# Optimization experiments

Measured on AMD Instinct MI355X. Metric: run time of the kernel, lower is better.

The kernel has to match this reference:

```python
import jax, jax.numpy as jnp
import numpy as np

B, T, D, H = 8, 2048, 256, 4
HD = D // H                      # head dim = 64
SCALE = float(np.sqrt(HD))       # math.sqrt(hd)
EPS = 1e-5                       # nn.LayerNorm default
NEG = -1e9                       # stand-in for -inf; sparsemax output identical (0)


def setup_inputs() -> dict:
    key = jax.random.key(0)
    ks = jax.random.split(key, 8)
    x = jax.random.normal(ks[0], (B, T, D), dtype=jnp.float32)
    key_padding_mask = jax.random.bernoulli(ks[1], 0.15, (B, T))
    w = lambda k: jax.random.normal(k, (D, D), dtype=jnp.float32) * 0.02
    return {
        "x": x,
        "key_padding_mask": key_padding_mask,
        "Wq": w(ks[2]), "Wk": w(ks[3]), "Wv": w(ks[4]), "Wo": w(ks[5]),
        "gamma": jnp.ones((D,), jnp.float32),
        "beta": jnp.zeros((D,), jnp.float32),
    }


def sparsemax(z):
    # exact sort-based sparsemax over last axis (Martins & Astudillo 2016)
    n = z.shape[-1]
    zs = -jnp.sort(-z, axis=-1)                      # descending
    k = jnp.arange(1, n + 1, dtype=z.dtype)
    cum = jnp.cumsum(zs, axis=-1)
    support = (1.0 + k * zs) > cum                   # k in support
    ksel = jnp.sum(support, axis=-1, keepdims=True)  # support size >= 1
    cum_k = jnp.take_along_axis(cum, ksel - 1, axis=-1)
    tau = (cum_k - 1.0) / ksel.astype(z.dtype)
    return jnp.maximum(z - tau, 0.0)


def _split(y):  # (B,T,D) -> (B,H,T,hd)
    return y.reshape(B, T, H, HD).transpose(0, 2, 1, 3)


def reference(x, key_padding_mask, Wq, Wk, Wv, Wo, gamma, beta):
    Q = _split(x @ Wq.T)
    K = _split(x @ Wk.T)
    V = _split(x @ Wv.T)
    scores = jnp.einsum('bhqd,bhkd->bhqk', Q, K) / SCALE     # (B,H,T,T)
    scores = jnp.where(key_padding_mask[:, None, None, :], NEG, scores)
    A = sparsemax(scores)
    out = jnp.einsum('bhqk,bhkd->bhqd', A, V)                # (B,H,T,hd)
    out = out.transpose(0, 2, 1, 3).reshape(B, T, D)
    y = out @ Wo.T + x                                       # out-proj + residual
    mu = jnp.mean(y, axis=-1, keepdims=True)
    var = jnp.mean(jnp.square(y - mu), axis=-1, keepdims=True)
    return (y - mu) / jnp.sqrt(var + EPS) * gamma + beta
```

## Files before the change

kernel.cpp:

```cpp
#include <hip/hip_runtime.h>

typedef unsigned short ushort_t;
typedef unsigned char uchar_t;

using bf16x8 = __attribute__((ext_vector_type(8))) short;
using f32x4  = __attribute__((ext_vector_type(4))) float;
using h2     = __attribute__((ext_vector_type(2))) _Float16;
using h8     = __attribute__((ext_vector_type(8))) _Float16;
using hc2    = __attribute__((ext_vector_type(2))) __fp16;
using hc8    = __attribute__((ext_vector_type(8))) __fp16;

#define B_  8
#define T_  2048
#define D_  256
#define H_  4
#define HD_ 64
#define BH_ (B_*H_)
#define M_  (B_*T_)

#define NX_   ((size_t)M_*D_)
#define NW_   ((size_t)D_*D_)
#define NCONV (NX_ + 4*NW_)

__device__ __forceinline__ float bf2f(ushort_t u) {
    union { unsigned int i; float f; } v; v.i = ((unsigned int)u) << 16; return v.f;
}
__device__ __forceinline__ ushort_t f2bf(float f) {
    union { float f; unsigned int i; } v; v.f = f;
    unsigned int u = v.i;
    u += 0x7FFFu + ((u >> 16) & 1u);
    return (ushort_t)(u >> 16);
}
__device__ __forceinline__ h2 pkh(float lo, float hi) {
    union { hc2 a; h2 b; } u;
    u.a = __builtin_amdgcn_cvt_pkrtz(lo, hi);
    return u.b;
}
__device__ __forceinline__ float dot2(h2 a, h2 b, float c) {
    union { h2 h; hc2 c2; } ua, ub; ua.h = a; ub.h = b;
    return __builtin_amdgcn_fdot2(ua.c2, ub.c2, c, false);
}
__device__ __forceinline__ f32x4 mfma_f16(h8 a, h8 b, f32x4 c) {
    union { h8 h; hc8 c8; } ua, ub; ua.h = a; ub.h = b;
    return __builtin_amdgcn_mfma_f32_16x16x32_f16(ua.c8, ub.c8, c, 0, 0, 0);
}
__device__ __forceinline__ f32x4 mfma_bf16(bf16x8 a, bf16x8 b, f32x4 c) {
    return __builtin_amdgcn_mfma_f32_16x16x32_bf16(a, b, c, 0, 0, 0);
}
__device__ __forceinline__ int is_bf16_inputs(const void* gamma) {
    return ((const unsigned int*)gamma)[0] == 0x3F803F80u;
}
union h2u { unsigned int u; int i; h2 h; };
union hu1 { _Float16 h; ushort_t u; };

__global__ __launch_bounds__(256) void conv_mask_kernel(
        const void* __restrict__ x,
        const void* __restrict__ Wq, const void* __restrict__ Wk,
        const void* __restrict__ Wv, const void* __restrict__ Wo,
        const void* __restrict__ gamma, ushort_t* __restrict__ dst,
        const uchar_t* __restrict__ mraw, ushort_t* __restrict__ mout) {
    int isbf = is_bf16_inputs(gamma);
    int tid = threadIdx.x;

    if (blockIdx.x < 16) {
        __shared__ int f_or1, f_ornz, f_max, cls;
        if (tid == 0) { f_or1 = 0; f_ornz = 0; f_max = 0; }
        __syncthreads();
        int lor1 = 0, lornz = 0, lmax = 0;
        for (int i = tid * 16; i < tid * 16 + 16; ++i) {
            int v = mraw[i];
            lmax = max(lmax, v);
            if ((i & 3) == 1) lor1 |= v;
            if ((i & 3) != 0) lornz |= v;
        }
        atomicOr(&f_or1, lor1); atomicOr(&f_ornz, lornz); atomicMax(&f_max, lmax);
        __syncthreads();
        if (tid == 0) {
            int c;
            if (f_max == 0)      c = 0;
            else if (f_max <= 1) c = f_ornz ? 0 : 1;
            else                 c = f_or1 ? 2 : 3;
            cls = c;
        }
        __syncthreads();
        int c = cls;
        int base = blockIdx.x * 1024;
        for (int e = base + tid; e < base + 1024; e += 256) {
            int m;
            if (c == 0)      m = mraw[e] != 0;
            else if (c == 1) m = ((const int*)mraw)[e] != 0;
            else if (c == 2) m = ((const ushort_t*)mraw)[e] != 0;
            else             m = ((const float*)mraw)[e] != 0.0f;
            hu1 cv; cv.h = m ? (_Float16)(-30000.0f) : (_Float16)0.0f;
            mout[e] = cv.u;
        }
    }

    size_t e = ((size_t)blockIdx.x * 256 + tid) * 8;
    if (e >= NCONV) return;
    const void* src; size_t off;
    if (e < NX_) { src = x; off = e; }
    else {
        size_t r = e - NX_; int wsel = (int)(r >> 16);
        src = (wsel == 0) ? Wq : (wsel == 1) ? Wk : (wsel == 2) ? Wv : Wo;
        off = r & 65535;
    }
    if (isbf) {
        *(bf16x8*)(dst + e) = *(const bf16x8*)((const ushort_t*)src + off);
    } else {
        const float4* s = (const float4*)((const float*)src + off);
        float4 a = s[0], b = s[1];
        ushort_t o8[8] = { f2bf(a.x), f2bf(a.y), f2bf(a.z), f2bf(a.w),
                           f2bf(b.x), f2bf(b.y), f2bf(b.z), f2bf(b.w) };
        *(bf16x8*)(dst + e) = *(bf16x8*)o8;
    }
}

__global__ __launch_bounds__(256) void qkv_kernel(
        const ushort_t* __restrict__ x,
        const ushort_t* __restrict__ Wq, const ushort_t* __restrict__ Wk,
        const ushort_t* __restrict__ Wv,
        ushort_t* __restrict__ Qs, ushort_t* __restrict__ Ks, ushort_t* __restrict__ Vt) {
    __shared__ __align__(16) ushort_t vtile[64][72];
    int mt = blockIdx.x, nt = blockIdx.y;
    int tid = threadIdx.x, w = tid >> 6, l = tid & 63, lr = l & 15, lg = l >> 4;
    int ncol0 = nt * 64 + w * 16;
    int mat = nt >> 2;
    int j0 = ncol0 & 255;
    const ushort_t* W = (mat == 0) ? Wq : ((mat == 1) ? Wk : Wv);
    const ushort_t* wrow  = W + (size_t)(j0 + lr) * 256 + lg * 8;
    const ushort_t* xbase = x + (size_t)(mt * 64 + lr) * 256 + lg * 8;

    f32x4 acc[4] = {};
    for (int kk = 0; kk < 256; kk += 32) {
        bf16x8 bfr = *(const bf16x8*)(wrow + kk);
        #pragma unroll
        for (int rt = 0; rt < 4; ++rt) {
            bf16x8 afr = *(const bf16x8*)(xbase + (size_t)rt * 16 * 256 + kk);
            acc[rt] = mfma_bf16(afr, bfr, acc[rt]);
        }
    }
    if (mat != 2) {
        int n = ncol0 + lr;
        int d = n & 255, h = d >> 6, hd = d & 63;
        ushort_t* dstm = (mat == 0) ? Qs : Ks;
        float scale = (mat == 0) ? 0.125f : 1.0f;
        #pragma unroll
        for (int rt = 0; rt < 4; ++rt) {
            #pragma unroll
            for (int r = 0; r < 4; ++r) {
                int i = mt * 64 + rt * 16 + lg * 4 + r;
                int b = i >> 11, t = i & (T_ - 1);
                int bh = b * H_ + h;
                union { _Float16 h; ushort_t u; } cv;
                cv.h = (_Float16)(acc[rt][r] * scale);
                dstm[((size_t)bh * T_ + t) * HD_ + hd] = cv.u;
            }
        }
    } else {
        int hd_l = w * 16 + lr;
        #pragma unroll
        for (int rt = 0; rt < 4; ++rt) {
            #pragma unroll
            for (int r = 0; r < 4; ++r) {
                union { _Float16 h; ushort_t u; } cv; cv.h = (_Float16)acc[rt][r];
                vtile[hd_l][rt * 16 + lg * 4 + r] = cv.u;
            }
        }
        __syncthreads();
        int hd2 = tid >> 2, seg = tid & 3;
        const uint4* src = (const uint4*)(&vtile[hd2][0]);
        uint4 a = src[seg * 2], b2 = src[seg * 2 + 1];
        int i0 = mt * 64;
        int bb2 = i0 >> 11, tb = i0 & (T_ - 1), h = nt - 8;
        size_t dstb = ((size_t)((bb2 * H_ + h) * HD_ + hd2)) * T_ + tb + seg * 16;
        *(uint4*)(Vt + dstb) = a;
        *(uint4*)(Vt + dstb + 8) = b2;
    }
}

__global__ __launch_bounds__(256, 2) void attn_kernel(
        const ushort_t* __restrict__ Qs, const ushort_t* __restrict__ Ks,
        const ushort_t* __restrict__ Vt, const ushort_t* __restrict__ biasbuf,
        ushort_t* __restrict__ attn_out) {
    __shared__ float red[512];
    __shared__ unsigned int obuf[2 * 4 * 16 * 33];
    int lin = blockIdx.y * (T_ / 32) + blockIdx.x;
    int work = (lin & 7) * 256 + (lin >> 3);
    int qt = work & 63, bh = work >> 6;
    int b = bh >> 2, h = bh & 3;
    int tid = threadIdx.x, w = tid >> 6, l = tid & 63, lr = l & 15, lg = l >> 4;

    const ushort_t* Qb = Qs + (size_t)bh * T_ * HD_;
    const ushort_t* Kb = Ks + (size_t)bh * T_ * HD_;
    const ushort_t* Vb = Vt + (size_t)bh * HD_ * T_;
    const ushort_t* brow = biasbuf + b * T_;

    const ushort_t* qrowA = Qb + (size_t)(qt * 32 + lr) * HD_ + lg * 8;
    h8 bqA0 = *(const h8*)(qrowA);
    h8 bqA1 = *(const h8*)(qrowA + 32);
    h8 bqB0 = *(const h8*)(qrowA + 16 * HD_);
    h8 bqB1 = *(const h8*)(qrowA + 16 * HD_ + 32);

    const int key_base = w * 512;
    const h2 hzero = { (_Float16)0.0f, (_Float16)0.0f };
    const h2 hone  = { (_Float16)1.0f, (_Float16)1.0f };
    const h2 hdlt  = { (_Float16)0.0078125f, (_Float16)0.0078125f };

    h2 scpA[64], scpB[64];
    h2 zmA = { (_Float16)(-30000.0f), (_Float16)(-30000.0f) };
    h2 zmB = zmA;
    const ushort_t* kp = Kb + (size_t)(key_base + lr) * HD_ + lg * 8;
    h8 ak0 = *(const h8*)(kp);
    h8 ak1 = *(const h8*)(kp + 32);
    #pragma unroll
    for (int i = 0; i < 32; ++i) {
        h8 nk0, nk1;
        if (i < 31) {
            const ushort_t* kn = kp + (size_t)(i + 1) * 16 * HD_;
            nk0 = *(const h8*)(kn);
            nk1 = *(const h8*)(kn + 32);
        }
        f32x4 cA = {}, cB = {};
        cA = mfma_f16(ak0, bqA0, cA);
        cB = mfma_f16(ak0, bqB0, cB);
        cA = mfma_f16(ak1, bqA1, cA);
        cB = mfma_f16(ak1, bqB1, cB);
        uint2 bm = *(const uint2*)(brow + key_base + i * 16 + lg * 4);
        h2u b01, b23; b01.u = bm.x; b23.u = bm.y;
        h2 pA0 = pkh(cA[0], cA[1]) + b01.h;
        h2 pA1 = pkh(cA[2], cA[3]) + b23.h;
        h2 pB0 = pkh(cB[0], cB[1]) + b01.h;
        h2 pB1 = pkh(cB[2], cB[3]) + b23.h;
        zmA = __builtin_elementwise_max(zmA, __builtin_elementwise_max(pA0, pA1));
        zmB = __builtin_elementwise_max(zmB, __builtin_elementwise_max(pB0, pB1));
        scpA[2 * i]     = pA0;
        scpA[2 * i + 1] = pA1;
        scpB[2 * i]     = pB0;
        scpB[2 * i + 1] = pB1;
        if (i < 31) { ak0 = nk0; ak1 = nk1; }
    }
    float zmaxA = fmaxf((float)zmA[0], (float)zmA[1]);
    float zmaxB = fmaxf((float)zmB[0], (float)zmB[1]);
    zmaxA = fmaxf(zmaxA, __shfl_xor(zmaxA, 16, 64));
    zmaxA = fmaxf(zmaxA, __shfl_xor(zmaxA, 32, 64));
    zmaxB = fmaxf(zmaxB, __shfl_xor(zmaxB, 16, 64));
    zmaxB = fmaxf(zmaxB, __shfl_xor(zmaxB, 32, 64));

    float zsA = -3e38f, zsB = -3e38f;
    #pragma unroll
    for (int j = 0; j < 8; ++j) {
        h2 pA = scpA[8 * j], pB = scpB[8 * j];
        zsA = fmaxf(zsA, fmaxf((float)pA[0], (float)pA[1]));
        zsB = fmaxf(zsB, fmaxf((float)pB[0], (float)pB[1]));
    }
    zsA = fmaxf(zsA, __shfl_xor(zsA, 16, 64));
    zsA = fmaxf(zsA, __shfl_xor(zsA, 32, 64));
    zsB = fmaxf(zsB, __shfl_xor(zsB, 16, 64));
    zsB = fmaxf(zsB, __shfl_xor(zsB, 32, 64));
    float twA = zsA - 1.0f, twB = zsB - 1.0f;
    #pragma unroll
    for (int it = 0; it < 6; ++it) {
        float thA = (float)(_Float16)twA, trA = twA - thA;
        float thB = (float)(_Float16)twB, trB = twB - thB;
        h2 t1A = pkh(thA, thA), t2A = pkh(trA, trA);
        h2 t1B = pkh(thB, thB), t2B = pkh(trB, trB);
        float SA = 0.0f, SmA = 0.0f, SB = 0.0f, SmB = 0.0f;
        #pragma unroll
        for (int j = 0; j < 8; ++j) {
            h2 dA = (scpA[8 * j] - t1A) - t2A;
            h2 dB = (scpB[8 * j] - t1B) - t2B;
            h2 mA = __builtin_elementwise_max(dA, hzero);
            h2 mB = __builtin_elementwise_max(dB, hzero);
            SA = dot2(mA, hone, SA);
            SB = dot2(mB, hone, SB);
            SmA = dot2(__builtin_elementwise_min(mA, hdlt), hone, SmA);
            SmB = dot2(__builtin_elementwise_min(mB, hdlt), hone, SmB);
        }
        SA += __shfl_xor(SA, 16, 64);  SA += __shfl_xor(SA, 32, 64);
        SB += __shfl_xor(SB, 16, 64);  SB += __shfl_xor(SB, 32, 64);
        SmA += __shfl_xor(SmA, 16, 64); SmA += __shfl_xor(SmA, 32, 64);
        SmB += __shfl_xor(SmB, 16, 64); SmB += __shfl_xor(SmB, 32, 64);
        float CA = fmaxf(SmA * 128.0f, 0.125f);
        float CB = fmaxf(SmB * 128.0f, 0.125f);
        twA += (SA - 0.03125f) / CA;
        twB += (SB - 0.03125f) / CB;
    }

    if (lg == 0) {
        red[w * 32 + lr * 2]       = twA;  red[w * 32 + lr * 2 + 1]       = zmaxA;
        red[128 + w * 32 + lr * 2] = twB;  red[128 + w * 32 + lr * 2 + 1] = zmaxB;
    }
    __syncthreads();
    float t4A = 0.25f * (red[lr * 2] + red[32 + lr * 2]
                       + red[64 + lr * 2] + red[96 + lr * 2]);
    float zbA = fmaxf(fmaxf(red[lr * 2 + 1], red[32 + lr * 2 + 1]),
                      fmaxf(red[64 + lr * 2 + 1], red[96 + lr * 2 + 1]));
    float t4B = 0.25f * (red[128 + lr * 2] + red[160 + lr * 2]
                       + red[192 + lr * 2] + red[224 + lr * 2]);
    float zbB = fmaxf(fmaxf(red[128 + lr * 2 + 1], red[160 + lr * 2 + 1]),
                      fmaxf(red[192 + lr * 2 + 1], red[224 + lr * 2 + 1]));
    float tauA = fminf(fmaxf(t4A, zbA - 1.0f), zbA - 0.01f);
    float tauB = fminf(fmaxf(t4B, zbB - 1.0f), zbB - 0.01f);

    int pp = 1;
    float tpA, tpB, SpA, SpB;
    bool done;
    {
        float thA = (float)(_Float16)tauA, trA = tauA - thA;
        float thB = (float)(_Float16)tauB, trB = tauB - thB;
        h2 t1A = pkh(thA, thA), t2A = pkh(trA, trA);
        h2 t1B = pkh(thB, thB), t2B = pkh(trB, trB);
        float SaA = 0.0f, SbA = 0.0f, CaA = 0.0f, CbA = 0.0f;
        float SaB = 0.0f, SbB = 0.0f, CaB = 0.0f, CbB = 0.0f;
        #pragma unroll
        for (int p2 = 0; p2 < 64; p2 += 2) {
            h2 mA0 = __builtin_elementwise_max((scpA[p2]     - t1A) - t2A, hzero);
            h2 mA1 = __builtin_elementwise_max((scpA[p2 + 1] - t1A) - t2A, hzero);
            h2 mB0 = __builtin_elementwise_max((scpB[p2]     - t1B) - t2B, hzero);
            h2 mB1 = __builtin_elementwise_max((scpB[p2 + 1] - t1B) - t2B, hzero);
            SaA = dot2(mA0, hone, SaA);
            SbA = dot2(mA1, hone, SbA);
            SaB = dot2(mB0, hone, SaB);
            SbB = dot2(mB1, hone, SbB);
            CaA = dot2(__builtin_elementwise_min(mA0, hdlt), hone, CaA);
            CbA = dot2(__builtin_elementwise_min(mA1, hdlt), hone, CbA);
            CaB = dot2(__builtin_elementwise_min(mB0, hdlt), hone, CaB);
            CbB = dot2(__builtin_elementwise_min(mB1, hdlt), hone, CbB);
        }
        float SA = SaA + SbA, SmA = CaA + CbA;
        float SB = SaB + SbB, SmB = CaB + CbB;
        SA += __shfl_xor(SA, 16, 64);   SA += __shfl_xor(SA, 32, 64);
        SB += __shfl_xor(SB, 16, 64);   SB += __shfl_xor(SB, 32, 64);
        SmA += __shfl_xor(SmA, 16, 64); SmA += __shfl_xor(SmA, 32, 64);
        SmB += __shfl_xor(SmB, 16, 64); SmB += __shfl_xor(SmB, 32, 64);
        float* rr = red + pp * 256;
        if (lg == 0) {
            float4 v4 = { SA, SmA, SB, SmB };
            *(float4*)&rr[w * 64 + lr * 4] = v4;
        }
        __syncthreads();
        float SAb = 0.0f, SmAb = 0.0f, SBb = 0.0f, SmBb = 0.0f;
        #pragma unroll
        for (int w2 = 0; w2 < 4; ++w2) {
            float4 v4 = *(const float4*)&rr[w2 * 64 + lr * 4];
            SAb += v4.x; SmAb += v4.y; SBb += v4.z; SmBb += v4.w;
        }
        float CA = fmaxf(SmAb * 128.0f, 1.0f);
        float CB = fmaxf(SmBb * 128.0f, 1.0f);
        float stepA = (SAb - 1.0f) / CA;
        float stepB = (SBb - 1.0f) / CB;
        tpA = tauA; SpA = SAb; tauA += stepA;
        tpB = tauB; SpB = SBb; tauB += stepB;
        pp ^= 1;
        done = __all(fmaxf(fabsf(stepA), fabsf(stepB)) < 2e-4f);
    }

    for (int it = 1; it < 6 && !done; ++it) {
        float thA = (float)(_Float16)tauA, trA = tauA - thA;
        float thB = (float)(_Float16)tauB, trB = tauB - thB;
        h2 t1A = pkh(thA, thA), t2A = pkh(trA, trA);
        h2 t1B = pkh(thB, thB), t2B = pkh(trB, trB);
        float SaA = 0.0f, SbA = 0.0f, SaB = 0.0f, SbB = 0.0f;
        #pragma unroll
        for (int p2 = 0; p2 < 64; p2 += 2) {
            h2 mA0 = __builtin_elementwise_max((scpA[p2]     - t1A) - t2A, hzero);
            h2 mA1 = __builtin_elementwise_max((scpA[p2 + 1] - t1A) - t2A, hzero);
            h2 mB0 = __builtin_elementwise_max((scpB[p2]     - t1B) - t2B, hzero);
            h2 mB1 = __builtin_elementwise_max((scpB[p2 + 1] - t1B) - t2B, hzero);
            SaA = dot2(mA0, hone, SaA);
            SbA = dot2(mA1, hone, SbA);
            SaB = dot2(mB0, hone, SaB);
            SbB = dot2(mB1, hone, SbB);
        }
        float SA = SaA + SbA, SB = SaB + SbB;
        SA += __shfl_xor(SA, 16, 64); SA += __shfl_xor(SA, 32, 64);
        SB += __shfl_xor(SB, 16, 64); SB += __shfl_xor(SB, 32, 64);
        float* rr = red + pp * 256;
        if (lg == 0) {
            float2 v2 = { SA, SB };
            *(float2*)&rr[w * 32 + lr * 2] = v2;
        }
        __syncthreads();
        float SAb = 0.0f, SBb = 0.0f;
        #pragma unroll
        for (int w2 = 0; w2 < 4; ++w2) {
            float2 v2 = *(const float2*)&rr[w2 * 32 + lr * 2];
            SAb += v2.x; SBb += v2.y;
        }
        float dA = tauA - tpA, dB = tauB - tpB;
        float CA = (fabsf(dA) > 1e-7f)
                 ? fminf(fmaxf((SpA - SAb) / dA, 1.0f), 1e7f) : 1e7f;
        float CB = (fabsf(dB) > 1e-7f)
                 ? fminf(fmaxf((SpB - SBb) / dB, 1.0f), 1e7f) : 1e7f;
        float stepA = (SAb - 1.0f) / CA;
        float stepB = (SBb - 1.0f) / CB;
        tpA = tauA; SpA = SAb; tauA += stepA;
        tpB = tauB; SpB = SBb; tauB += stepB;
        pp ^= 1;
        done = __all(fmaxf(fabsf(stepA), fabsf(stepB)) < 2e-4f);
    }

    float thA = (float)(_Float16)tauA, trA = tauA - thA;
    float thB = (float)(_Float16)tauB, trB = tauB - thB;
    h2 t1A = pkh(thA, thA), t2A = pkh(trA, trA);
    h2 t1B = pkh(thB, thB), t2B = pkh(trB, trB);
    int idxA = 4 * (lr + 32 * (lg & 1));
    int idxB = idxA + 64;
    bool hi2 = (lg >> 1) != 0;
    f32x4 accA0 = {}, accA1 = {}, accA2 = {}, accA3 = {};
    f32x4 accB0 = {}, accB1 = {}, accB2 = {}, accB3 = {};
    const ushort_t* vb2 = Vb + (size_t)lr * T_ + key_base + lg * 8;
    h8 va0 = *(const h8*)(vb2);
    h8 va1 = *(const h8*)(vb2 + (size_t)16 * T_);
    h8 va2 = *(const h8*)(vb2 + (size_t)32 * T_);
    h8 va3 = *(const h8*)(vb2 + (size_t)48 * T_);
    #pragma unroll
    for (int c = 0; c < 16; ++c) {
        h8 na0, na1, na2, na3;
        if (c < 15) {
            const ushort_t* vp = vb2 + (c + 1) * 32;
            na0 = *(const h8*)(vp);
            na1 = *(const h8*)(vp + (size_t)16 * T_);
            na2 = *(const h8*)(vp + (size_t)32 * T_);
            na3 = *(const h8*)(vp + (size_t)48 * T_);
        }
        h2u pA0, pA1, pA2, pA3, pB0, pB1, pB2, pB3;
        pA0.h = __builtin_elementwise_max((scpA[4*c]   - t1A) - t2A, hzero);
        pA1.h = __builtin_elementwise_max((scpA[4*c+1] - t1A) - t2A, hzero);
        pA2.h = __builtin_elementwise_max((scpA[4*c+2] - t1A) - t2A, hzero);
        pA3.h = __builtin_elementwise_max((scpA[4*c+3] - t1A) - t2A, hzero);
        pB0.h = __builtin_elementwise_max((scpB[4*c]   - t1B) - t2B, hzero);
        pB1.h = __builtin_elementwise_max((scpB[4*c+1] - t1B) - t2B, hzero);
        pB2.h = __builtin_elementwise_max((scpB[4*c+2] - t1B) - t2B, hzero);
        pB3.h = __builtin_elementwise_max((scpB[4*c+3] - t1B) - t2B, hzero);
        int wAA0  = __builtin_amdgcn_ds_bpermute(idxA, pA0.i);
        int wAA0o = __builtin_amdgcn_ds_bpermute(idxA, pA2.i);
        int wAA1  = __builtin_amdgcn_ds_bpermute(idxA, pA1.i);
        int wAA1o = __builtin_amdgcn_ds_bpermute(idxA, pA3.i);
        int wAB0  = __builtin_amdgcn_ds_bpermute(idxB, pA0.i);
        int wAB0o = __builtin_amdgcn_ds_bpermute(idxB, pA2.i);
        int wAB1  = __builtin_amdgcn_ds_bpermute(idxB, pA1.i);
        int wAB1o = __builtin_amdgcn_ds_bpermute(idxB, pA3.i);
        int wBA0  = __builtin_amdgcn_ds_bpermute(idxA, pB0.i);
        int wBA0o = __builtin_amdgcn_ds_bpermute(idxA, pB2.i);
        int wBA1  = __builtin_amdgcn_ds_bpermute(idxA, pB1.i);
        int wBA1o = __builtin_amdgcn_ds_bpermute(idxA, pB3.i);
        int wBB0  = __builtin_amdgcn_ds_bpermute(idxB, pB0.i);
        int wBB0o = __builtin_amdgcn_ds_bpermute(idxB, pB2.i);
        int wBB1  = __builtin_amdgcn_ds_bpermute(idxB, pB1.i);
        int wBB1o = __builtin_amdgcn_ds_bpermute(idxB, pB3.i);
        union { int u[4]; h8 v8; } bbA, bbB;
        bbA.u[0] = hi2 ? wAA0o : wAA0;
        bbA.u[1] = hi2 ? wAA1o : wAA1;
        bbA.u[2] = hi2 ? wAB0o : wAB0;
        bbA.u[3] = hi2 ? wAB1o : wAB1;
        bbB.u[0] = hi2 ? wBA0o : wBA0;
        bbB.u[1] = hi2 ? wBA1o : wBA1;
        bbB.u[2] = hi2 ? wBB0o : wBB0;
        bbB.u[3] = hi2 ? wBB1o : wBB1;
        accA0 = mfma_f16(va0, bbA.v8, accA0);
        accB0 = mfma_f16(va0, bbB.v8, accB0);
        accA1 = mfma_f16(va1, bbA.v8, accA1);
        accB1 = mfma_f16(va1, bbB.v8, accB1);
        accA2 = mfma_f16(va2, bbA.v8, accA2);
        accB2 = mfma_f16(va2, bbB.v8, accB2);
        accA3 = mfma_f16(va3, bbA.v8, accA3);
        accB3 = mfma_f16(va3, bbB.v8, accB3);
        if (c < 15) { va0 = na0; va1 = na1; va2 = na2; va3 = na3; }
    }

    {
        int ob = w * 528 + lr * 33;
        h2u e0, e1, e2, e3, e4, e5, e6, e7;
        e0.h = pkh(accA0[0], accA0[1]); e1.h = pkh(accA0[2], accA0[3]);
        e2.h = pkh(accA1[0], accA1[1]); e3.h = pkh(accA1[2], accA1[3]);
        e4.h = pkh(accA2[0], accA2[1]); e5.h = pkh(accA2[2], accA2[3]);
        e6.h = pkh(accA3[0], accA3[1]); e7.h = pkh(accA3[2], accA3[3]);
        obuf[ob + 2 * lg]          = e0.u;
        obuf[ob + 2 * lg + 1]      = e1.u;
        obuf[ob + 8 + 2 * lg]      = e2.u;
        obuf[ob + 8 + 2 * lg + 1]  = e3.u;
        obuf[ob + 16 + 2 * lg]     = e4.u;
        obuf[ob + 16 + 2 * lg + 1] = e5.u;
        obuf[ob + 24 + 2 * lg]     = e6.u;
        obuf[ob + 24 + 2 * lg + 1] = e7.u;
        int ob2 = 2112 + ob;
        e0.h = pkh(accB0[0], accB0[1]); e1.h = pkh(accB0[2], accB0[3]);
        e2.h = pkh(accB1[0], accB1[1]); e3.h = pkh(accB1[2], accB1[3]);
        e4.h = pkh(accB2[0], accB2[1]); e5.h = pkh(accB2[2], accB2[3]);
        e6.h = pkh(accB3[0], accB3[1]); e7.h = pkh(accB3[2], accB3[3]);
        obuf[ob2 + 2 * lg]          = e0.u;
        obuf[ob2 + 2 * lg + 1]      = e1.u;
        obuf[ob2 + 8 + 2 * lg]      = e2.u;
        obuf[ob2 + 8 + 2 * lg + 1]  = e3.u;
        obuf[ob2 + 16 + 2 * lg]     = e4.u;
        obuf[ob2 + 16 + 2 * lg + 1] = e5.u;
        obuf[ob2 + 24 + 2 * lg]     = e6.u;
        obuf[ob2 + 24 + 2 * lg + 1] = e7.u;
    }
    __syncthreads();
    int hd = tid & 63;
    #pragma unroll
    for (int k = 0; k < 4; ++k) {
        int row = (tid >> 6) * 4 + k;
        float vA = 0.0f, vB = 0.0f;
        #pragma unroll
        for (int w2 = 0; w2 < 4; ++w2) {
            h2u pA; pA.u = obuf[w2 * 528 + row * 33 + (hd >> 1)];
            h2u pB; pB.u = obuf[2112 + w2 * 528 + row * 33 + (hd >> 1)];
            vA += (float)pA.h[hd & 1];
            vB += (float)pB.h[hd & 1];
        }
        int tgA = qt * 32 + row;
        int tgB = tgA + 16;
        attn_out[((size_t)(b * T_ + tgA)) * D_ + h * HD_ + hd] = f2bf(vA);
        attn_out[((size_t)(b * T_ + tgB)) * D_ + h * HD_ + hd] = f2bf(vB);
    }
}

__global__ __launch_bounds__(256, 2) void oproj_ln_kernel(
        const ushort_t* __restrict__ ao, const ushort_t* __restrict__ Wo,
        const void* __restrict__ xres, const void* __restrict__ gamma,
        const void* __restrict__ beta, void* __restrict__ out) {
    __shared__ float psum[4][32][2];
    int isbf = is_bf16_inputs(gamma);
    int mt = blockIdx.x;
    int tid = threadIdx.x, w = tid >> 6, l = tid & 63, lr = l & 15, lg = l >> 4;
    const ushort_t* abase = ao + (size_t)(mt * 32 + lr) * 256 + lg * 8;
    const ushort_t* wbase = Wo + (size_t)(w * 64 + lr) * 256 + lg * 8;

    f32x4 acc[2][4] = {};
    for (int kk = 0; kk < 256; kk += 32) {
        bf16x8 bfr[4];
        #pragma unroll
        for (int ct = 0; ct < 4; ++ct)
            bfr[ct] = *(const bf16x8*)(wbase + (size_t)ct * 16 * 256 + kk);
        #pragma unroll
        for (int rt = 0; rt < 2; ++rt) {
            bf16x8 afr = *(const bf16x8*)(abase + (size_t)rt * 16 * 256 + kk);
            #pragma unroll
            for (int ct = 0; ct < 4; ++ct)
                acc[rt][ct] = mfma_bf16(afr, bfr[ct], acc[rt][ct]);
        }
    }

    #pragma unroll
    for (int rt = 0; rt < 2; ++rt) {
        #pragma unroll
        for (int r = 0; r < 4; ++r) {
            int row = rt * 16 + lg * 4 + r;
            size_t gro = (size_t)(mt * 32 + row) * 256;
            float s = 0.0f, s2 = 0.0f;
            #pragma unroll
            for (int ct = 0; ct < 4; ++ct) {
                int col = w * 64 + ct * 16 + lr;
                float xr = isbf ? bf2f(((const ushort_t*)xres)[gro + col])
                                : ((const float*)xres)[gro + col];
                float yv = acc[rt][ct][r] + xr;
                acc[rt][ct][r] = yv;
                s += yv; s2 += yv * yv;
            }
            #pragma unroll
            for (int o = 1; o < 16; o <<= 1) {
                s  += __shfl_xor(s, o, 64);
                s2 += __shfl_xor(s2, o, 64);
            }
            if (lr == 0) { psum[w][row][0] = s; psum[w][row][1] = s2; }
        }
    }
    __syncthreads();

    float gv[4], bv[4];
    #pragma unroll
    for (int ct = 0; ct < 4; ++ct) {
        int col = w * 64 + ct * 16 + lr;
        gv[ct] = isbf ? bf2f(((const ushort_t*)gamma)[col]) : ((const float*)gamma)[col];
        bv[ct] = isbf ? bf2f(((const ushort_t*)beta)[col])  : ((const float*)beta)[col];
    }
    #pragma unroll
    for (int rt = 0; rt < 2; ++rt) {
        #pragma unroll
        for (int r = 0; r < 4; ++r) {
            int row = rt * 16 + lg * 4 + r;
            float S  = psum[0][row][0] + psum[1][row][0]
                     + psum[2][row][0] + psum[3][row][0];
            float S2 = psum[0][row][1] + psum[1][row][1]
                     + psum[2][row][1] + psum[3][row][1];
            float mean = S * (1.0f / 256.0f);
            float var  = S2 * (1.0f / 256.0f) - mean * mean;
            float rstd = rsqrtf(var + 1e-5f);
            size_t gro = (size_t)(mt * 32 + row) * 256;
            #pragma unroll
            for (int ct = 0; ct < 4; ++ct) {
                int col = w * 64 + ct * 16 + lr;
                float o = (acc[rt][ct][r] - mean) * rstd * gv[ct] + bv[ct];
                if (isbf) ((ushort_t*)out)[gro + col] = f2bf(o);
                else      ((float*)out)[gro + col] = o;
            }
        }
    }
}

extern "C" void kernel_launch(void* const* d_in, const int* in_sizes, int n_in,
                              void* d_out, int out_size, void* d_ws, size_t ws_size,
                              hipStream_t stream) {
    const void*     x     = d_in[0];
    const uchar_t*  mraw  = (const uchar_t*)d_in[1];
    const void*     Wq    = d_in[2];
    const void*     Wk    = d_in[3];
    const void*     Wv    = d_in[4];
    const void*     Wo    = d_in[5];
    const void*     gamma = d_in[6];
    const void*     beta  = d_in[7];

    char* ws = (char*)d_ws;
    const size_t OFF_XB   = 0;
    const size_t OFF_WB   = 8388608;
    const size_t OFF_QS   = 9437184;
    const size_t OFF_KS   = OFF_QS + 8388608;
    const size_t OFF_VT   = OFF_KS + 8388608;
    const size_t OFF_MB   = OFF_VT + 8388608;
    if (ws_size < OFF_MB + 32768) return;

    ushort_t* xb   = (ushort_t*)(ws + OFF_XB);
    ushort_t* Wqb  = (ushort_t*)(ws + OFF_WB);
    ushort_t* Wkb  = Wqb + NW_;
    ushort_t* Wvb  = Wkb + NW_;
    ushort_t* Wob  = Wvb + NW_;
    ushort_t* Qs   = (ushort_t*)(ws + OFF_QS);
    ushort_t* Ks   = (ushort_t*)(ws + OFF_KS);
    ushort_t* Vt   = (ushort_t*)(ws + OFF_VT);
    ushort_t* ao   = (ushort_t*)(ws + OFF_XB);
    ushort_t* mbuf = (ushort_t*)(ws + OFF_MB);

    conv_mask_kernel<<<(int)(NCONV / 8 / 256), 256, 0, stream>>>(
        x, Wq, Wk, Wv, Wo, gamma, xb, mraw, mbuf);
    qkv_kernel<<<dim3(M_ / 64, 12), 256, 0, stream>>>(xb, Wqb, Wkb, Wvb, Qs, Ks, Vt);
    attn_kernel<<<dim3(T_ / 32, BH_), 256, 0, stream>>>(Qs, Ks, Vt, mbuf, ao);
    oproj_ln_kernel<<<M_ / 32, 256, 0, stream>>>(ao, Wob, x, gamma, beta, d_out);
}
```

Before: 316.7 us.

## Retile QKV projection to 32x256 blocks and stage Q/K stores through LDS

```diff
diff --git a/kernel.cpp b/kernel.cpp
--- a/kernel.cpp
+++ b/kernel.cpp
@@ -121,61 +121,77 @@
         const ushort_t* __restrict__ Wq, const ushort_t* __restrict__ Wk,
         const ushort_t* __restrict__ Wv,
         ushort_t* __restrict__ Qs, ushort_t* __restrict__ Ks, ushort_t* __restrict__ Vt) {
-    __shared__ __align__(16) ushort_t vtile[64][72];
-    int mt = blockIdx.x, nt = blockIdx.y;
+    __shared__ __align__(16) ushort_t vtile[10240];
+    int mt = blockIdx.x, mat = blockIdx.y;
     int tid = threadIdx.x, w = tid >> 6, l = tid & 63, lr = l & 15, lg = l >> 4;
-    int ncol0 = nt * 64 + w * 16;
-    int mat = nt >> 2;
-    int j0 = ncol0 & 255;
     const ushort_t* W = (mat == 0) ? Wq : ((mat == 1) ? Wk : Wv);
-    const ushort_t* wrow  = W + (size_t)(j0 + lr) * 256 + lg * 8;
-    const ushort_t* xbase = x + (size_t)(mt * 64 + lr) * 256 + lg * 8;
-
-    f32x4 acc[4] = {};
+    const ushort_t* wbase = W + (size_t)(w * 64 + lr) * 256 + lg * 8;
+    const ushort_t* xbase = x + (size_t)(mt * 32 + lr) * 256 + lg * 8;
+
+    f32x4 acc[2][4] = {};
     for (int kk = 0; kk < 256; kk += 32) {
-        bf16x8 bfr = *(const bf16x8*)(wrow + kk);
-        #pragma unroll
-        for (int rt = 0; rt < 4; ++rt) {
+        bf16x8 bfr[4];
+        #pragma unroll
+        for (int ct = 0; ct < 4; ++ct)
+            bfr[ct] = *(const bf16x8*)(wbase + (size_t)ct * 16 * 256 + kk);
+        #pragma unroll
+        for (int rt = 0; rt < 2; ++rt) {
             bf16x8 afr = *(const bf16x8*)(xbase + (size_t)rt * 16 * 256 + kk);
-            acc[rt] = mfma_bf16(afr, bfr, acc[rt]);
-        }
-    }
+            #pragma unroll
+            for (int ct = 0; ct < 4; ++ct)
+                acc[rt][ct] = mfma_bf16(afr, bfr[ct], acc[rt][ct]);
+        }
+    }
+
+    int b = mt >> 6, t0 = (mt * 32) & (T_ - 1);
     if (mat != 2) {
-        int n = ncol0 + lr;
-        int d = n & 255, h = d >> 6, hd = d & 63;
-        ushort_t* dstm = (mat == 0) ? Qs : Ks;
         float scale = (mat == 0) ? 0.125f : 1.0f;
         #pragma unroll
-        for (int rt = 0; rt < 4; ++rt) {
+        for (int rt = 0; rt < 2; ++rt) {
             #pragma unroll
             for (int r = 0; r < 4; ++r) {
-                int i = mt * 64 + rt * 16 + lg * 4 + r;
-                int b = i >> 11, t = i & (T_ - 1);
-                int bh = b * H_ + h;
-                union { _Float16 h; ushort_t u; } cv;
-                cv.h = (_Float16)(acc[rt][r] * scale);
-                dstm[((size_t)bh * T_ + t) * HD_ + hd] = cv.u;
+                int row = rt * 16 + lg * 4 + r;
+                #pragma unroll
+                for (int ct = 0; ct < 4; ++ct) {
+                    int col = w * 64 + ct * 16 + lr;
+                    hu1 cv; cv.h = (_Float16)(acc[rt][ct][r] * scale);
+                    vtile[row * 264 + col] = cv.u;
+                }
             }
         }
+        __syncthreads();
+        ushort_t* dstm = (mat == 0) ? Qs : Ks;
+        #pragma unroll
+        for (int k = 0; k < 4; ++k) {
+            int idx = tid + k * 256;
+            int row = idx >> 5, seg = idx & 31;
+            uint4 v = *(const uint4*)&vtile[row * 264 + seg * 8];
+            int head = seg >> 3, hd0 = (seg & 7) * 8;
+            *(uint4*)(dstm + ((size_t)((b * H_ + head) * T_ + t0 + row)) * HD_ + hd0) = v;
+        }
     } else {
-        int hd_l = w * 16 + lr;
-        #pragma unroll
-        for (int rt = 0; rt < 4; ++rt) {
+        #pragma unroll
+        for (int rt = 0; rt < 2; ++rt) {
             #pragma unroll
             for (int r = 0; r < 4; ++r) {
-                union { _Float16 h; ushort_t u; } cv; cv.h = (_Float16)acc[rt][r];
-                vtile[hd_l][rt * 16 + lg * 4 + r] = cv.u;
+                int row = rt * 16 + lg * 4 + r;
+                #pragma unroll
+                for (int ct = 0; ct < 4; ++ct) {
+                    int col = w * 64 + ct * 16 + lr;
+                    hu1 cv; cv.h = (_Float16)acc[rt][ct][r];
+                    vtile[col * 40 + row] = cv.u;
+                }
             }
         }
         __syncthreads();
-        int hd2 = tid >> 2, seg = tid & 3;
-        const uint4* src = (const uint4*)(&vtile[hd2][0]);
-        uint4 a = src[seg * 2], b2 = src[seg * 2 + 1];
-        int i0 = mt * 64;
-        int bb2 = i0 >> 11, tb = i0 & (T_ - 1), h = nt - 8;
-        size_t dstb = ((size_t)((bb2 * H_ + h) * HD_ + hd2)) * T_ + tb + seg * 16;
-        *(uint4*)(Vt + dstb) = a;
-        *(uint4*)(Vt + dstb + 8) = b2;
+        #pragma unroll
+        for (int k = 0; k < 4; ++k) {
+            int idx = tid + k * 256;
+            int d = idx >> 2, seg = idx & 3;
+            uint4 v = *(const uint4*)&vtile[d * 40 + seg * 8];
+            int head = d >> 6, hd = d & 63;
+            *(uint4*)(Vt + ((size_t)((b * H_ + head) * HD_ + hd)) * T_ + t0 + seg * 8) = v;
+        }
     }
 }
 
@@ -636,7 +652,7 @@
 
     conv_mask_kernel<<<(int)(NCONV / 8 / 256), 256, 0, stream>>>(
         x, Wq, Wk, Wv, Wo, gamma, xb, mraw, mbuf);
-    qkv_kernel<<<dim3(M_ / 64, 12), 256, 0, stream>>>(xb, Wqb, Wkb, Wvb, Qs, Ks, Vt);
+    qkv_kernel<<<dim3(M_ / 32, 3), 256, 0, stream>>>(xb, Wqb, Wkb, Wvb, Qs, Ks, Vt);
     attn_kernel<<<dim3(T_ / 32, BH_), 256, 0, stream>>>(Qs, Ks, Vt, mbuf, ao);
     oproj_ln_kernel<<<M_ / 32, 256, 0, stream>>>(ao, Wob, x, gamma, beta, d_out);
 }
```

Result: faster. 295.0 us (-6.9%).
